# Kernel optimization log

Measured on AMD Instinct MI355X. Metric: run time of the kernel, lower is better.

## Reference

```python
import jax, jax.numpy as jnp
import numpy as np


def _pano_affinity():
    # Faithful port of get_pano_affinity(): 3 rings of 12 views, 3x3 Gaussian
    # blur (cv2 ksize=3 sigma=0 => sigma=0.8), BORDER_TRANSPARENT (borders kept),
    # diagonal reset to 1; zeros replaced by 0.01 as done in __init__.
    p = np.eye(36, dtype=np.float64)
    for v in range(12):  # top ring
        p[v, v + 12] = 1
        l = (v - 1) % 12
        r = (v + 1) % 12
        p[v, l] = 1; p[v, l + 12] = 1
        p[v, r] = 1; p[v, r + 12] = 1
    for v in range(12, 24):  # middle ring
        p[v, v + 12] = 1; p[v, v - 12] = 1
        l = (v - 13) % 12 + 12
        r = (v - 11) % 12 + 12
        p[v, l] = 1; p[v, l + 12] = 1; p[v, l - 12] = 1
        p[v, r] = 1; p[v, r + 12] = 1; p[v, r - 12] = 1
    for v in range(24, 36):  # bottom ring
        p[v, v - 12] = 1
        l = (v - 25) % 12 + 24
        r = (v - 23) % 12 + 24
        p[v, l] = 1; p[v, l - 12] = 1
        p[v, r] = 1; p[v, r - 12] = 1
    assert np.sum(p - p.T) == 0
    kern = np.exp(-np.array([-1.0, 0.0, 1.0]) ** 2 / (2 * 0.8 ** 2))
    kern /= kern.sum()
    a, b = kern[0], kern[1]
    t = a * p[:, :-2] + b * p[:, 1:-1] + a * p[:, 2:]
    t2 = a * t[:-2, :] + b * t[1:-1, :] + a * t[2:, :]
    out = p.copy()
    out[1:-1, 1:-1] = t2  # transparent border: edge pixels unblurred
    out[np.eye(36, dtype=bool)] = 1.0
    out[out == 0] = 0.01
    return out.astype(np.float32)


def _ln(x, g, b):
    mu = jnp.mean(x, -1, keepdims=True)
    v = jnp.mean(jnp.square(x - mu), -1, keepdims=True)
    return (x - mu) * jax.lax.rsqrt(v + 1e-5) * g + b


def setup_inputs() -> dict:
    key = jax.random.key(0)
    ks = jax.random.split(key, 12)
    B, L, V, D, KD, KV, Q, H = 128, 36, 36, 512, 300, 112, 36, 512
    s = 0.02
    return {
        'h': jax.random.normal(ks[0], (B, Q), jnp.float32),
        'context': jax.random.normal(ks[1], (B, L, V, D), jnp.float32),
        'teacher_action_view_ids': jax.random.randint(ks[2], (B,), 0, 36),
        'detect_feats': jax.random.normal(ks[3], (B, L, KD), jnp.float32),
        'knowledge_vector': jax.random.normal(ks[4], (B, L, KV), jnp.float32),
        'pano_a': jnp.asarray(_pano_affinity()),
        'W_q': jax.random.normal(ks[5], (Q, Q), jnp.float32) * s,
        'W_k': jax.random.normal(ks[6], (Q, D + KD), jnp.float32) * s,
        'gru_Wih': jax.random.normal(ks[7], (3 * Q, D + KV), jnp.float32) * s,
        'gru_Whh': jax.random.normal(ks[8], (3 * Q, Q), jnp.float32) * s,
        'gru_bih': jnp.zeros((3 * Q,), jnp.float32),
        'gru_bhh': jnp.zeros((3 * Q,), jnp.float32),
        'ln_slots_g': jnp.ones((Q,), jnp.float32),
        'ln_slots_b': jnp.zeros((Q,), jnp.float32),
        'ln_ff_g': jnp.ones((Q,), jnp.float32),
        'ln_ff_b': jnp.zeros((Q,), jnp.float32),
        'mlp_W1': jax.random.normal(ks[9], (H, Q), jnp.float32) * s,
        'mlp_b1': jnp.zeros((H,), jnp.float32),
        'mlp_W2': jax.random.normal(ks[10], (Q, H), jnp.float32) * s,
        'mlp_b2': jnp.zeros((Q,), jnp.float32),
    }


def reference(h, context, teacher_action_view_ids, detect_feats, knowledge_vector,
              pano_a, W_q, W_k, gru_Wih, gru_Whh, gru_bih, gru_bhh,
              ln_slots_g, ln_slots_b, ln_ff_g, ln_ff_b,
              mlp_W1, mlp_b1, mlp_W2, mlp_b2):
    B, L, V, D = context.shape
    Q = pano_a.shape[0]  # 36
    scale = Q ** -0.5
    iters = 3
    slots = jnp.broadcast_to(pano_a, (B, Q, Q))
    # context_know = cat(context, detect_feats broadcast over 36 views)
    ck = jnp.concatenate(
        [context, jnp.broadcast_to(detect_feats[:, :, None, :], (B, L, V, detect_feats.shape[-1]))], axis=-1)
    k = jnp.einsum('bljc,qc->bljq', ck, W_k)  # [B,L,36,Q]
    attn_ws = []
    for _ in range(iters):
        slots_prev = slots
        q = jnp.einsum('bie,qe->biq', _ln(slots, ln_slots_g, ln_slots_b), W_q)  # [B,Q,Q]
        dots = jnp.einsum('bid,bkjd->bkj', q, k) * scale  # i summed out, as in source
        attn = jax.nn.softmax(dots, axis=-1)  # softmax over views
        attn_ws.append(attn)
        updates = jnp.einsum('bkjd,bij->bid', context, attn)  # [B,L,D]
        x = jnp.concatenate([updates, knowledge_vector], axis=-1).reshape(-1, D + knowledge_vector.shape[-1])
        hp = slots_prev.reshape(-1, Q)
        # torch.nn.GRUCell (gate order r, z, n)
        gx = x @ gru_Wih.T + gru_bih
        gh = hp @ gru_Whh.T + gru_bhh
        xr, xz, xn = jnp.split(gx, 3, axis=-1)
        hr, hz, hn = jnp.split(gh, 3, axis=-1)
        r = jax.nn.sigmoid(xr + hr)
        z = jax.nn.sigmoid(xz + hz)
        n = jnp.tanh(xn + r * hn)
        gnew = ((1.0 - z) * n + z * hp).reshape(B, -1, Q)
        ff = _ln(gnew, ln_ff_g, ln_ff_b)
        gnew = gnew + (jax.nn.relu(ff @ mlp_W1.T + mlp_b1) @ mlp_W2.T + mlp_b2)
        slots = gnew
    return slots, jnp.stack(attn_ws, 0)
```

## Files before the change

kernel.cpp:

```cpp
#include <hip/hip_runtime.h>

namespace {
constexpr int Bc = 128, Lc = 36, Vc = 36, Dc = 512, KDc = 300, KVc = 112, Qc = 36, Hc = 512;
constexpr int ROWS = Bc * Lc * Vc;
constexpr int BLn  = Bc * Lc;
constexpr int SLOT = Bc * Qc * Qc;
constexpr float SCALE = 1.0f / 6.0f;
}

__device__ __forceinline__ float wave_sum(float v) {
  #pragma unroll
  for (int off = 32; off > 0; off >>= 1) v += __shfl_xor(v, off, 64);
  return v;
}
__device__ __forceinline__ float wave_max(float v) {
  #pragma unroll
  for (int off = 32; off > 0; off >>= 1) v = fmaxf(v, __shfl_xor(v, off, 64));
  return v;
}
__device__ __forceinline__ float sigmoidf_(float x) { return 1.f / (1.f + __expf(-x)); }

__global__ __launch_bounds__(256) void csum_kernel(const float* __restrict__ ctx, float* __restrict__ csum) {
  int tid = blockIdx.x * 256 + threadIdx.x;
  int b  = tid / (Vc * Dc);
  int jd = tid % (Vc * Dc);
  const float* p = ctx + (size_t)b * Lc * Vc * Dc + jd;
  float s = 0.f;
  #pragma unroll
  for (int l = 0; l < Lc; ++l) s += p[(size_t)l * (Vc * Dc)];
  csum[tid] = s;
}

__global__ void kd_kernel(const float* __restrict__ det, const float* __restrict__ Wk,
                          float* __restrict__ kd) {
  __shared__ float ds[KDc];
  int bl = blockIdx.x; int t = threadIdx.x;
  for (int c = t; c < KDc; c += 64) ds[c] = det[(size_t)bl * KDc + c];
  __syncthreads();
  if (t < Qc) {
    const float* w = Wk + (size_t)t * 812 + 512;
    float acc = 0.f;
    #pragma unroll 4
    for (int c = 0; c < KDc; ++c) acc = fmaf(ds[c], w[c], acc);
    kd[(size_t)bl * Qc + t] = acc;
  }
}

__global__ __launch_bounds__(256) void k_gemm(const float* __restrict__ A, const float* __restrict__ Wk,
                       const float* __restrict__ kd, float* __restrict__ kout) {
  __shared__ __align__(16) float As[32 * 260];
  __shared__ __align__(16) float Bs[32 * 48];
  int t = threadIdx.x;
  int rb = blockIdx.x * 256;
  int tr = t & 63, tc = t >> 6;
  float acc[4][9];
  #pragma unroll
  for (int i = 0; i < 4; ++i)
    #pragma unroll
    for (int c = 0; c < 9; ++c) acc[i][c] = 0.f;

  for (int d0 = 0; d0 < 512; d0 += 32) {
    #pragma unroll
    for (int jj = 0; jj < 8; ++jj) {
      int idx = t + jj * 256;
      int kkb = (idx & 7) * 4, r = idx >> 3;
      const float4 v = *(const float4*)(A + (size_t)(rb + r) * 512 + d0 + kkb);
      As[(kkb + 0) * 260 + r] = v.x;
      As[(kkb + 1) * 260 + r] = v.y;
      As[(kkb + 2) * 260 + r] = v.z;
      As[(kkb + 3) * 260 + r] = v.w;
    }
    for (int idx = t; idx < 32 * 36; idx += 256) {
      int kk = idx / 36, c = idx % 36;
      Bs[kk * 48 + (c / 9) * 12 + (c % 9)] = Wk[(size_t)c * 812 + d0 + kk];
    }
    __syncthreads();
    #pragma unroll
    for (int kk = 0; kk < 32; ++kk) {
      const float4 a  = *(const float4*)&As[kk * 260 + tr * 4];
      const float* bp = &Bs[kk * 48 + tc * 12];
      const float4 b0 = *(const float4*)bp;
      const float4 b1 = *(const float4*)(bp + 4);
      const float  b8 = bp[8];
      const float av[4] = {a.x, a.y, a.z, a.w};
      const float bv[9] = {b0.x, b0.y, b0.z, b0.w, b1.x, b1.y, b1.z, b1.w, b8};
      #pragma unroll
      for (int i = 0; i < 4; ++i)
        #pragma unroll
        for (int c = 0; c < 9; ++c) acc[i][c] = fmaf(av[i], bv[c], acc[i][c]);
    }
    __syncthreads();
  }
  #pragma unroll
  for (int i = 0; i < 4; ++i) {
    int row = rb + tr * 4 + i;
    int bl = row / 36;
    #pragma unroll
    for (int c = 0; c < 9; ++c) {
      int q = tc * 9 + c;
      kout[(size_t)row * 36 + q] = acc[i][c] + kd[(size_t)bl * 36 + q];
    }
  }
}

__global__ __launch_bounds__(256) void prew_gemm(const float* __restrict__ A, int lda, int K, int k0,
                                                 const float* __restrict__ Wih, float* __restrict__ outp) {
  __shared__ __align__(16) float As[16 * 68];
  __shared__ __align__(16) float Bs[16 * 112];
  int t = threadIdx.x;
  int rb = blockIdx.x * 64;
  int tr = t & 63, tc = t >> 6;
  float acc[27];
  #pragma unroll
  for (int c = 0; c < 27; ++c) acc[c] = 0.f;

  for (int kk0 = 0; kk0 < K; kk0 += 16) {
    {
      int r = t >> 2, kq = (t & 3) * 4;
      const float4 v = *(const float4*)(A + (size_t)(rb + r) * lda + kk0 + kq);
      As[(kq + 0) * 68 + r] = v.x;
      As[(kq + 1) * 68 + r] = v.y;
      As[(kq + 2) * 68 + r] = v.z;
      As[(kq + 3) * 68 + r] = v.w;
    }
    for (int idx = t; idx < 16 * 108; idx += 256) {
      int k = idx / 108, c = idx % 108;
      Bs[k * 112 + (c / 27) * 28 + (c % 27)] = Wih[(size_t)c * 624 + k0 + kk0 + k];
    }
    __syncthreads();
    #pragma unroll
    for (int k = 0; k < 16; ++k) {
      const float a = As[k * 68 + tr];
      const float* bp = &Bs[k * 112 + tc * 28];
      float bv[27];
      #pragma unroll
      for (int c4 = 0; c4 < 6; ++c4) {
        float4 b4 = *(const float4*)(bp + c4 * 4);
        bv[c4 * 4 + 0] = b4.x; bv[c4 * 4 + 1] = b4.y; bv[c4 * 4 + 2] = b4.z; bv[c4 * 4 + 3] = b4.w;
      }
      bv[24] = bp[24]; bv[25] = bp[25]; bv[26] = bp[26];
      #pragma unroll
      for (int c = 0; c < 27; ++c) acc[c] = fmaf(a, bv[c], acc[c]);
    }
    __syncthreads();
  }
  int row = rb + tr;
  #pragma unroll
  for (int c = 0; c < 27; ++c)
    outp[(size_t)row * 108 + tc * 27 + c] = acc[c];
}

__global__ __launch_bounds__(256) void mega_kernel(
    const float* __restrict__ pano, const float* __restrict__ kmat,
    const float* __restrict__ cw,   const float* __restrict__ gknw,
    const float* __restrict__ Wq,   const float* __restrict__ Whh,
    const float* __restrict__ bih,  const float* __restrict__ bhh,
    const float* __restrict__ lsg,  const float* __restrict__ lsb,
    const float* __restrict__ lfg,  const float* __restrict__ lfb,
    const float* __restrict__ W1,   const float* __restrict__ b1,
    const float* __restrict__ W2,   const float* __restrict__ b2,
    float* __restrict__ out) {
  const int b = blockIdx.x;
  const int t = threadIdx.x;
  const int wv = t >> 6, lane = t & 63;

  __shared__ float s0[36 * 37], s1[36 * 37];
  __shared__ float at[36 * 36];
  __shared__ float cw_s[36 * 108], gk_s[36 * 108];
  __shared__ float whh_s[108 * 37];
  __shared__ float ff_s[36 * 37];
  __shared__ float ls4[192];
  __shared__ float qs[36];
  __shared__ __align__(16) float wst[128 * 37];
  __shared__ __align__(16) float mid_s[36 * 132];

  for (int idx = t; idx < 1296; idx += 256) s0[(idx / 36) * 37 + idx % 36] = pano[idx];
  for (int idx = t; idx < 3888; idx += 256) {
    cw_s[idx] = cw[(size_t)b * 3888 + idx];
    gk_s[idx] = gknw[(size_t)b * 3888 + idx];
    whh_s[(idx / 36) * 37 + idx % 36] = Whh[idx];
  }
  float gv = 0.f, bv = 0.f, fg = 0.f, fb = 0.f, b2v = 0.f;
  if (lane < 36) { gv = lsg[lane]; bv = lsb[lane]; fg = lfg[lane]; fb = lfb[lane]; b2v = b2[lane]; }
  const float* kb = kmat + (size_t)b * 1296 * 36;
  __syncthreads();

  #pragma unroll
  for (int it = 0; it < 3; ++it) {
    float* cur = (it == 1) ? s1 : s0;
    float* nxt = (it == 1) ? s0 : s1;
    float* aout = out + SLOT + (size_t)it * SLOT + (size_t)b * 1296;

    float lnsum = 0.f;
    #pragma unroll
    for (int ii = 0; ii < 9; ++ii) {
      int i = wv + 4 * ii;
      float x = (lane < 36) ? cur[i * 37 + lane] : 0.f;
      float mu = wave_sum(x) * (1.f / 36.f);
      float d = x - mu;
      float var = wave_sum((lane < 36) ? d * d : 0.f) * (1.f / 36.f);
      float ln = d * rsqrtf(var + 1e-5f) * gv + bv;
      if (lane < 36) lnsum += ln;
    }
    if (lane < 36) ls4[wv * 37 + lane] = lnsum;
    __syncthreads();
    if (t < 36) {
      float l0 = ls4[t] + ls4[37 + t] + ls4[74 + t] + ls4[111 + t];
      ls4[148 + t] = l0;
    }
    if (t < 36) {
      float acc = 0.f;
      #pragma unroll
      for (int e = 0; e < 36; ++e) acc = fmaf(ls4[148 + e], Wq[t * 36 + e], acc);
      qs[t] = acc;
    }
    __syncthreads();

    #pragma unroll
    for (int ii = 0; ii < 9; ++ii) {
      int l = wv * 9 + ii;
      float dot = 0.f;
      if (lane < 36) {
        const float* kp = kb + ((size_t)l * 36 + lane) * 36;
        #pragma unroll
        for (int c = 0; c < 9; ++c) {
          float4 kv = *(const float4*)(kp + 4 * c);
          dot += kv.x * qs[4 * c] + kv.y * qs[4 * c + 1] + kv.z * qs[4 * c + 2] + kv.w * qs[4 * c + 3];
        }
      }
      dot *= SCALE;
      float m = wave_max((lane < 36) ? dot : -1e30f);
      float e = (lane < 36) ? __expf(dot - m) : 0.f;
      float s = wave_sum(e);
      if (lane < 36) {
        float a = e / s;
        at[l * 36 + lane] = a;
        aout[(size_t)l * 36 + lane] = a;
      }
    }
    __syncthreads();

    for (int idx = t; idx < 1296; idx += 256) {
      int i = idx / 36, c = idx % 36;
      const float* ar = &at[i * 36];
      float xr = gk_s[i * 108 + c]      + bih[c];
      float xz = gk_s[i * 108 + 36 + c] + bih[36 + c];
      float xn = gk_s[i * 108 + 72 + c] + bih[72 + c];
      #pragma unroll 4
      for (int j = 0; j < 36; ++j) {
        float a = ar[j];
        xr = fmaf(a, cw_s[j * 108 + c],      xr);
        xz = fmaf(a, cw_s[j * 108 + 36 + c], xz);
        xn = fmaf(a, cw_s[j * 108 + 72 + c], xn);
      }
      float hr = bhh[c], hz = bhh[36 + c], hn = bhh[72 + c];
      const float* hrow = &cur[i * 37];
      #pragma unroll 4
      for (int e = 0; e < 36; ++e) {
        float h = hrow[e];
        hr = fmaf(h, whh_s[c * 37 + e],        hr);
        hz = fmaf(h, whh_s[(36 + c) * 37 + e], hz);
        hn = fmaf(h, whh_s[(72 + c) * 37 + e], hn);
      }
      float r = sigmoidf_(xr + hr), z = sigmoidf_(xz + hz);
      float n = tanhf(xn + r * hn);
      nxt[i * 37 + c] = (1.f - z) * n + z * hrow[c];
    }
    __syncthreads();

    #pragma unroll
    for (int ii = 0; ii < 9; ++ii) {
      int i = wv * 9 + ii;
      float v = (lane < 36) ? nxt[i * 37 + lane] : 0.f;
      float mu = wave_sum(v) * (1.f / 36.f);
      float d = v - mu;
      float var = wave_sum((lane < 36) ? d * d : 0.f) * (1.f / 36.f);
      float rstd = rsqrtf(var + 1e-5f);
      if (lane < 36) {
        ff_s[i * 37 + lane] = d * rstd * fg + fb;
        nxt[i * 37 + lane] = v + b2v;
      }
    }
    __syncthreads();

    float acc[6] = {0.f, 0.f, 0.f, 0.f, 0.f, 0.f};
    for (int h0 = 0; h0 < 512; h0 += 128) {
      for (int idx = t; idx < 4608; idx += 256)
        wst[(idx / 36) * 37 + idx % 36] = W1[(size_t)h0 * 36 + idx];
      __syncthreads();
      for (int idx = t; idx < 4608; idx += 256) {
        int i = idx >> 7, hh = idx & 127;
        float a = b1[h0 + hh];
        const float* fr = &ff_s[i * 37];
        const float* wr = &wst[hh * 37];
        #pragma unroll 4
        for (int e = 0; e < 36; ++e) a = fmaf(fr[e], wr[e], a);
        mid_s[i * 132 + hh] = fmaxf(a, 0.f);
      }
      __syncthreads();
      for (int idx = t; idx < 4608; idx += 256)
        wst[(idx >> 7) * 129 + (idx & 127)] = W2[(size_t)(idx >> 7) * 512 + h0 + (idx & 127)];
      __syncthreads();
      #pragma unroll
      for (int pi = 0; pi < 6; ++pi) {
        int idx = t + pi * 256;
        if (idx < 1296) {
          int i = idx / 36, c = idx % 36;
          const float* mr = &mid_s[i * 132];
          const float* wr = &wst[c * 129];
          float a = acc[pi];
          #pragma unroll 4
          for (int hh = 0; hh < 128; ++hh) a = fmaf(mr[hh], wr[hh], a);
          acc[pi] = a;
        }
      }
      __syncthreads();
    }
    #pragma unroll
    for (int pi = 0; pi < 6; ++pi) {
      int idx = t + pi * 256;
      if (idx < 1296) nxt[(idx / 36) * 37 + idx % 36] += acc[pi];
    }
    __syncthreads();
  }

  for (int idx = t; idx < 1296; idx += 256)
    out[(size_t)b * 1296 + idx] = s1[(idx / 36) * 37 + idx % 36];
}

extern "C" void kernel_launch(void* const* d_in, const int* in_sizes, int n_in,
                              void* d_out, int out_size, void* d_ws, size_t ws_size,
                              hipStream_t stream) {
  const float* ctx  = (const float*)d_in[1];
  const float* det  = (const float*)d_in[3];
  const float* knw  = (const float*)d_in[4];
  const float* pano = (const float*)d_in[5];
  const float* Wq   = (const float*)d_in[6];
  const float* Wk   = (const float*)d_in[7];
  const float* Wih  = (const float*)d_in[8];
  const float* Whh  = (const float*)d_in[9];
  const float* bih  = (const float*)d_in[10];
  const float* bhh  = (const float*)d_in[11];
  const float* lsg  = (const float*)d_in[12];
  const float* lsb  = (const float*)d_in[13];
  const float* lfg  = (const float*)d_in[14];
  const float* lfb  = (const float*)d_in[15];
  const float* W1   = (const float*)d_in[16];
  const float* b1   = (const float*)d_in[17];
  const float* W2   = (const float*)d_in[18];
  const float* b2   = (const float*)d_in[19];
  float* out = (float*)d_out;

  float* w = (float*)d_ws;
  float* kmat = w; w += (size_t)ROWS * 36;
  float* csum = w; w += (size_t)Bc * Vc * Dc;
  float* kd   = w; w += (size_t)BLn * Qc;
  float* cw   = w; w += (size_t)BLn * 108;
  float* gknw = w; w += (size_t)BLn * 108;

  csum_kernel<<<(Bc * Vc * Dc) / 256, 256, 0, stream>>>(ctx, csum);
  kd_kernel<<<BLn, 64, 0, stream>>>(det, Wk, kd);
  k_gemm<<<ROWS / 256, 256, 0, stream>>>(ctx, Wk, kd, kmat);
  prew_gemm<<<72, 256, 0, stream>>>(csum, 512, 512, 0,   Wih, cw);
  prew_gemm<<<72, 256, 0, stream>>>(knw,  112, 112, 512, Wih, gknw);
  mega_kernel<<<Bc, 256, 0, stream>>>(pano, kmat, cw, gknw, Wq, Whh, bih, bhh,
                                      lsg, lsb, lfg, lfb, W1, b1, W2, b2, out);
}
```

Measured before the change: 1.178 ms.

## Register-tile GRU and MLP in mega kernel, widen to 512 threads

The per-batch recurrent kernel now runs with 512 threads. Its GRU and MLP matmuls compute 2x2 or 3x4 output tiles per thread with float4 shared-memory loads, which gives more register reuse. The kernel drops the shared-memory staging of W1/W2 and reads those weights directly from global memory (cache), and pads smem rows to 40/44 floats for aligned vector loads. The aim is to shorten the serial mega_kernel, which runs only 128 blocks. In exchange it uses more registers per thread and makes uncoalesced, cache-dependent global weight reads.

```diff
diff --git a/kernel.cpp b/kernel.cpp
--- a/kernel.cpp
+++ b/kernel.cpp
@@ -19,6 +19,9 @@
   return v;
 }
 __device__ __forceinline__ float sigmoidf_(float x) { return 1.f / (1.f + __expf(-x)); }
+__device__ __forceinline__ float dot4_(float4 a, float4 b) {
+  return fmaf(a.x, b.x, fmaf(a.y, b.y, fmaf(a.z, b.z, a.w * b.w)));
+}
 
 __global__ __launch_bounds__(256) void csum_kernel(const float* __restrict__ ctx, float* __restrict__ csum) {
   int tid = blockIdx.x * 256 + threadIdx.x;
@@ -150,7 +153,7 @@
     outp[(size_t)row * 108 + tc * 27 + c] = acc[c];
 }
 
-__global__ __launch_bounds__(256) void mega_kernel(
+__global__ __launch_bounds__(512) void mega_kernel(
     const float* __restrict__ pano, const float* __restrict__ kmat,
     const float* __restrict__ cw,   const float* __restrict__ gknw,
     const float* __restrict__ Wq,   const float* __restrict__ Whh,
@@ -164,28 +167,28 @@
   const int t = threadIdx.x;
   const int wv = t >> 6, lane = t & 63;
 
-  __shared__ float s0[36 * 37], s1[36 * 37];
+  __shared__ __align__(16) float s0[36 * 40], s1[36 * 40];
   __shared__ float at[36 * 36];
-  __shared__ float cw_s[36 * 108], gk_s[36 * 108];
-  __shared__ float whh_s[108 * 37];
-  __shared__ float ff_s[36 * 37];
-  __shared__ float ls4[192];
+  __shared__ __align__(16) float cw_s[36 * 108], gk_s[36 * 108];
+  __shared__ __align__(16) float whh_s[108 * 44];
+  __shared__ __align__(16) float ff_s[36 * 40];
+  __shared__ float ls8[8 * 37];
   __shared__ float qs[36];
-  __shared__ __align__(16) float wst[128 * 37];
   __shared__ __align__(16) float mid_s[36 * 132];
 
-  for (int idx = t; idx < 1296; idx += 256) s0[(idx / 36) * 37 + idx % 36] = pano[idx];
-  for (int idx = t; idx < 3888; idx += 256) {
-    cw_s[idx] = cw[(size_t)b * 3888 + idx];
-    gk_s[idx] = gknw[(size_t)b * 3888 + idx];
-    whh_s[(idx / 36) * 37 + idx % 36] = Whh[idx];
-  }
+  for (int q4 = t; q4 < 972; q4 += 512) {
+    *(float4*)&cw_s[q4 * 4] = *(const float4*)(cw   + (size_t)b * 3888 + q4 * 4);
+    *(float4*)&gk_s[q4 * 4] = *(const float4*)(gknw + (size_t)b * 3888 + q4 * 4);
+  }
+  for (int idx = t; idx < 3888; idx += 512)
+    whh_s[(idx / 36) * 44 + idx % 36] = Whh[idx];
+  for (int idx = t; idx < 1296; idx += 512)
+    s0[(idx / 36) * 40 + idx % 36] = pano[idx];
   float gv = 0.f, bv = 0.f, fg = 0.f, fb = 0.f, b2v = 0.f;
   if (lane < 36) { gv = lsg[lane]; bv = lsb[lane]; fg = lfg[lane]; fb = lfb[lane]; b2v = b2[lane]; }
   const float* kb = kmat + (size_t)b * 1296 * 36;
   __syncthreads();
 
-  #pragma unroll
   for (int it = 0; it < 3; ++it) {
     float* cur = (it == 1) ? s1 : s0;
     float* nxt = (it == 1) ? s0 : s1;
@@ -193,139 +196,194 @@
 
     float lnsum = 0.f;
     #pragma unroll
-    for (int ii = 0; ii < 9; ++ii) {
-      int i = wv + 4 * ii;
-      float x = (lane < 36) ? cur[i * 37 + lane] : 0.f;
+    for (int ii = 0; ii < 5; ++ii) {
+      int i = wv + 8 * ii;
+      bool act = (i < 36) && (lane < 36);
+      float x = act ? cur[i * 40 + lane] : 0.f;
       float mu = wave_sum(x) * (1.f / 36.f);
       float d = x - mu;
-      float var = wave_sum((lane < 36) ? d * d : 0.f) * (1.f / 36.f);
+      float var = wave_sum(act ? d * d : 0.f) * (1.f / 36.f);
       float ln = d * rsqrtf(var + 1e-5f) * gv + bv;
-      if (lane < 36) lnsum += ln;
-    }
-    if (lane < 36) ls4[wv * 37 + lane] = lnsum;
+      if (act) lnsum += ln;
+    }
+    if (lane < 36) ls8[wv * 37 + lane] = lnsum;
     __syncthreads();
     if (t < 36) {
-      float l0 = ls4[t] + ls4[37 + t] + ls4[74 + t] + ls4[111 + t];
-      ls4[148 + t] = l0;
-    }
+      float l0 = 0.f;
+      #pragma unroll
+      for (int w = 0; w < 8; ++w) l0 += ls8[w * 37 + t];
+      ls8[8 * 37 - 37 + t] = 0.f;
+      float acc = 0.f;
+      ls8[296 - 296 + t] = l0;
+    }
+    __syncthreads();
     if (t < 36) {
       float acc = 0.f;
       #pragma unroll
-      for (int e = 0; e < 36; ++e) acc = fmaf(ls4[148 + e], Wq[t * 36 + e], acc);
+      for (int e = 0; e < 36; ++e) acc = fmaf(ls8[e], Wq[t * 36 + e], acc);
       qs[t] = acc;
     }
     __syncthreads();
 
     #pragma unroll
-    for (int ii = 0; ii < 9; ++ii) {
-      int l = wv * 9 + ii;
-      float dot = 0.f;
-      if (lane < 36) {
-        const float* kp = kb + ((size_t)l * 36 + lane) * 36;
-        #pragma unroll
-        for (int c = 0; c < 9; ++c) {
-          float4 kv = *(const float4*)(kp + 4 * c);
-          dot += kv.x * qs[4 * c] + kv.y * qs[4 * c + 1] + kv.z * qs[4 * c + 2] + kv.w * qs[4 * c + 3];
-        }
-      }
-      dot *= SCALE;
-      float m = wave_max((lane < 36) ? dot : -1e30f);
-      float e = (lane < 36) ? __expf(dot - m) : 0.f;
-      float s = wave_sum(e);
-      if (lane < 36) {
-        float a = e / s;
-        at[l * 36 + lane] = a;
-        aout[(size_t)l * 36 + lane] = a;
-      }
-    }
-    __syncthreads();
-
-    for (int idx = t; idx < 1296; idx += 256) {
-      int i = idx / 36, c = idx % 36;
-      const float* ar = &at[i * 36];
-      float xr = gk_s[i * 108 + c]      + bih[c];
-      float xz = gk_s[i * 108 + 36 + c] + bih[36 + c];
-      float xn = gk_s[i * 108 + 72 + c] + bih[72 + c];
+    for (int ii = 0; ii < 5; ++ii) {
+      int l = wv + 8 * ii;
+      if (l < 36) {
+        float dot = 0.f;
+        if (lane < 36) {
+          const float* kp = kb + ((size_t)l * 36 + lane) * 36;
+          #pragma unroll
+          for (int c = 0; c < 9; ++c) {
+            float4 kv = *(const float4*)(kp + 4 * c);
+            dot += kv.x * qs[4 * c] + kv.y * qs[4 * c + 1] + kv.z * qs[4 * c + 2] + kv.w * qs[4 * c + 3];
+          }
+        }
+        dot *= SCALE;
+        float m = wave_max((lane < 36) ? dot : -1e30f);
+        float e = (lane < 36) ? __expf(dot - m) : 0.f;
+        float s = wave_sum(e);
+        if (lane < 36) {
+          float a = e / s;
+          at[l * 36 + lane] = a;
+          aout[(size_t)l * 36 + lane] = a;
+        }
+      }
+    }
+    __syncthreads();
+
+    if (t < 324) {
+      int i0 = (t / 18) * 2, c0 = (t % 18) * 2;
+      float ax[3][2][2], ah[3][2][2];
+      #pragma unroll
+      for (int g = 0; g < 3; ++g)
+        #pragma unroll
+        for (int r = 0; r < 2; ++r)
+          #pragma unroll
+          for (int cc = 0; cc < 2; ++cc) {
+            ax[g][r][cc] = gk_s[(i0 + r) * 108 + g * 36 + c0 + cc] + bih[g * 36 + c0 + cc];
+            ah[g][r][cc] = bhh[g * 36 + c0 + cc];
+          }
       #pragma unroll 4
       for (int j = 0; j < 36; ++j) {
-        float a = ar[j];
-        xr = fmaf(a, cw_s[j * 108 + c],      xr);
-        xz = fmaf(a, cw_s[j * 108 + 36 + c], xz);
-        xn = fmaf(a, cw_s[j * 108 + 72 + c], xn);
-      }
-      float hr = bhh[c], hz = bhh[36 + c], hn = bhh[72 + c];
-      const float* hrow = &cur[i * 37];
-      #pragma unroll 4
-      for (int e = 0; e < 36; ++e) {
-        float h = hrow[e];
-        hr = fmaf(h, whh_s[c * 37 + e],        hr);
-        hz = fmaf(h, whh_s[(36 + c) * 37 + e], hz);
-        hn = fmaf(h, whh_s[(72 + c) * 37 + e], hn);
-      }
-      float r = sigmoidf_(xr + hr), z = sigmoidf_(xz + hz);
-      float n = tanhf(xn + r * hn);
-      nxt[i * 37 + c] = (1.f - z) * n + z * hrow[c];
-    }
-    __syncthreads();
-
-    #pragma unroll
-    for (int ii = 0; ii < 9; ++ii) {
-      int i = wv * 9 + ii;
-      float v = (lane < 36) ? nxt[i * 37 + lane] : 0.f;
-      float mu = wave_sum(v) * (1.f / 36.f);
-      float d = v - mu;
-      float var = wave_sum((lane < 36) ? d * d : 0.f) * (1.f / 36.f);
-      float rstd = rsqrtf(var + 1e-5f);
-      if (lane < 36) {
-        ff_s[i * 37 + lane] = d * rstd * fg + fb;
-        nxt[i * 37 + lane] = v + b2v;
-      }
-    }
-    __syncthreads();
-
-    float acc[6] = {0.f, 0.f, 0.f, 0.f, 0.f, 0.f};
+        float a0 = at[i0 * 36 + j], a1 = at[(i0 + 1) * 36 + j];
+        #pragma unroll
+        for (int g = 0; g < 3; ++g)
+          #pragma unroll
+          for (int cc = 0; cc < 2; ++cc) {
+            float wjc = cw_s[j * 108 + g * 36 + c0 + cc];
+            ax[g][0][cc] = fmaf(a0, wjc, ax[g][0][cc]);
+            ax[g][1][cc] = fmaf(a1, wjc, ax[g][1][cc]);
+          }
+      }
+      #pragma unroll
+      for (int eq = 0; eq < 9; ++eq) {
+        float4 h0q = *(const float4*)&cur[i0 * 40 + eq * 4];
+        float4 h1q = *(const float4*)&cur[(i0 + 1) * 40 + eq * 4];
+        #pragma unroll
+        for (int g = 0; g < 3; ++g)
+          #pragma unroll
+          for (int cc = 0; cc < 2; ++cc) {
+            float4 wq4 = *(const float4*)&whh_s[(g * 36 + c0 + cc) * 44 + eq * 4];
+            ah[g][0][cc] += dot4_(h0q, wq4);
+            ah[g][1][cc] += dot4_(h1q, wq4);
+          }
+      }
+      #pragma unroll
+      for (int r = 0; r < 2; ++r)
+        #pragma unroll
+        for (int cc = 0; cc < 2; ++cc) {
+          int i = i0 + r, c = c0 + cc;
+          float hp = cur[i * 40 + c];
+          float rr = sigmoidf_(ax[0][r][cc] + ah[0][r][cc]);
+          float zz = sigmoidf_(ax[1][r][cc] + ah[1][r][cc]);
+          float nn = tanhf(ax[2][r][cc] + rr * ah[2][r][cc]);
+          nxt[i * 40 + c] = (1.f - zz) * nn + zz * hp;
+        }
+    }
+    __syncthreads();
+
+    #pragma unroll
+    for (int ii = 0; ii < 5; ++ii) {
+      int i = wv + 8 * ii;
+      if (i < 36) {
+        float v = (lane < 36) ? nxt[i * 40 + lane] : 0.f;
+        float mu = wave_sum(v) * (1.f / 36.f);
+        float d = v - mu;
+        float var = wave_sum((lane < 36) ? d * d : 0.f) * (1.f / 36.f);
+        float rstd = rsqrtf(var + 1e-5f);
+        if (lane < 36) {
+          ff_s[i * 40 + lane] = d * rstd * fg + fb;
+          nxt[i * 40 + lane] = v + b2v;
+        }
+      }
+    }
+    __syncthreads();
+
+    float acc2[2][2] = {{0.f, 0.f}, {0.f, 0.f}};
     for (int h0 = 0; h0 < 512; h0 += 128) {
-      for (int idx = t; idx < 4608; idx += 256)
-        wst[(idx / 36) * 37 + idx % 36] = W1[(size_t)h0 * 36 + idx];
+      if (t < 384) {
+        int ig = t >> 5, hq = t & 31;
+        int i_0 = ig * 3;
+        int hh = h0 + hq * 4;
+        float4 bq = *(const float4*)&b1[hh];
+        float m[3][4] = {{bq.x, bq.y, bq.z, bq.w},
+                         {bq.x, bq.y, bq.z, bq.w},
+                         {bq.x, bq.y, bq.z, bq.w}};
+        const float* w1p = W1 + (size_t)hh * 36;
+        #pragma unroll
+        for (int eq = 0; eq < 9; ++eq) {
+          float4 f0 = *(const float4*)&ff_s[i_0 * 40 + eq * 4];
+          float4 f1 = *(const float4*)&ff_s[(i_0 + 1) * 40 + eq * 4];
+          float4 f2 = *(const float4*)&ff_s[(i_0 + 2) * 40 + eq * 4];
+          #pragma unroll
+          for (int c = 0; c < 4; ++c) {
+            float4 wq4 = *(const float4*)(w1p + (size_t)c * 36 + eq * 4);
+            m[0][c] += dot4_(f0, wq4);
+            m[1][c] += dot4_(f1, wq4);
+            m[2][c] += dot4_(f2, wq4);
+          }
+        }
+        #pragma unroll
+        for (int r = 0; r < 3; ++r) {
+          float4 o;
+          o.x = fmaxf(m[r][0], 0.f); o.y = fmaxf(m[r][1], 0.f);
+          o.z = fmaxf(m[r][2], 0.f); o.w = fmaxf(m[r][3], 0.f);
+          *(float4*)&mid_s[(i_0 + r) * 132 + hq * 4] = o;
+        }
+      }
       __syncthreads();
-      for (int idx = t; idx < 4608; idx += 256) {
-        int i = idx >> 7, hh = idx & 127;
-        float a = b1[h0 + hh];
-        const float* fr = &ff_s[i * 37];
-        const float* wr = &wst[hh * 37];
-        #pragma unroll 4
-        for (int e = 0; e < 36; ++e) a = fmaf(fr[e], wr[e], a);
-        mid_s[i * 132 + hh] = fmaxf(a, 0.f);
+      if (t < 324) {
+        int i0 = (t / 18) * 2, c0 = (t % 18) * 2;
+        const float* w2a = W2 + (size_t)c0 * 512 + h0;
+        const float* w2b = W2 + (size_t)(c0 + 1) * 512 + h0;
+        #pragma unroll 8
+        for (int kq = 0; kq < 32; ++kq) {
+          float4 m0 = *(const float4*)&mid_s[i0 * 132 + kq * 4];
+          float4 m1 = *(const float4*)&mid_s[(i0 + 1) * 132 + kq * 4];
+          float4 w0 = *(const float4*)(w2a + kq * 4);
+          float4 w1 = *(const float4*)(w2b + kq * 4);
+          acc2[0][0] += dot4_(m0, w0);
+          acc2[0][1] += dot4_(m0, w1);
+          acc2[1][0] += dot4_(m1, w0);
+          acc2[1][1] += dot4_(m1, w1);
+        }
       }
       __syncthreads();
-      for (int idx = t; idx < 4608; idx += 256)
-        wst[(idx >> 7) * 129 + (idx & 127)] = W2[(size_t)(idx >> 7) * 512 + h0 + (idx & 127)];
-      __syncthreads();
-      #pragma unroll
-      for (int pi = 0; pi < 6; ++pi) {
-        int idx = t + pi * 256;
-        if (idx < 1296) {
-          int i = idx / 36, c = idx % 36;
-          const float* mr = &mid_s[i * 132];
-          const float* wr = &wst[c * 129];
-          float a = acc[pi];
-          #pragma unroll 4
-          for (int hh = 0; hh < 128; ++hh) a = fmaf(mr[hh], wr[hh], a);
-          acc[pi] = a;
-        }
-      }
-      __syncthreads();
-    }
-    #pragma unroll
-    for (int pi = 0; pi < 6; ++pi) {
-      int idx = t + pi * 256;
-      if (idx < 1296) nxt[(idx / 36) * 37 + idx % 36] += acc[pi];
-    }
-    __syncthreads();
-  }
-
-  for (int idx = t; idx < 1296; idx += 256)
-    out[(size_t)b * 1296 + idx] = s1[(idx / 36) * 37 + idx % 36];
+    }
+    if (t < 324) {
+      int i0 = (t / 18) * 2, c0 = (t % 18) * 2;
+      nxt[i0 * 40 + c0]             += acc2[0][0];
+      nxt[i0 * 40 + c0 + 1]         += acc2[0][1];
+      nxt[(i0 + 1) * 40 + c0]       += acc2[1][0];
+      nxt[(i0 + 1) * 40 + c0 + 1]   += acc2[1][1];
+    }
+    __syncthreads();
+  }
+
+  for (int v4 = t; v4 < 324; v4 += 512) {
+    int row = v4 / 9, q = v4 % 9;
+    *(float4*)&out[(size_t)b * 1296 + row * 36 + q * 4] = *(const float4*)&s1[row * 40 + q * 4];
+  }
 }
 
 extern "C" void kernel_launch(void* const* d_in, const int* in_sizes, int n_in,
@@ -363,6 +421,6 @@
   k_gemm<<<ROWS / 256, 256, 0, stream>>>(ctx, Wk, kd, kmat);
   prew_gemm<<<72, 256, 0, stream>>>(csum, 512, 512, 0,   Wih, cw);
   prew_gemm<<<72, 256, 0, stream>>>(knw,  112, 112, 512, Wih, gknw);
-  mega_kernel<<<Bc, 256, 0, stream>>>(pano, kmat, cw, gknw, Wq, Whh, bih, bhh,
+  mega_kernel<<<Bc, 512, 0, stream>>>(pano, kmat, cw, gknw, Wq, Whh, bih, bhh,
                                       lsg, lsb, lfg, lfb, W1, b1, W2, b2, out);
 }
```

New measurement: 1.104 ms. -6.3%, faster.
